# Performance work log

Measured on AMD Instinct MI355X. Metric: run time of the kernel, lower is better.

The kernel has to match this reference:

```python
import jax, jax.numpy as jnp
import numpy as np

B, T, C, L = 256, 256, 1024, 32
NEG = -1e30   # log-domain 'zero'
EPS = 1e-7    # keras.backend.epsilon()


def setup_inputs() -> dict:
    key = jax.random.key(0)
    k1, k2 = jax.random.split(key)
    # ctc_batch_cost expects softmax probabilities
    y_pred = jax.nn.softmax(jax.random.normal(k1, (B, T, C), dtype=jnp.float32), axis=-1)
    # labels in [1, C-2]: 0 is padding (count_nonzero), C-1 is the CTC blank
    y_true = jax.random.randint(k2, (B, L), 1, C - 1).astype(jnp.int32)
    return {"y_true": y_true, "y_pred": y_pred}


def _ctc_batch_cost(y_true, y_pred):
    b, t, c = y_pred.shape
    blank = c - 1                                   # TF ctc_loss: blank = last class
    lp = jnp.log(y_pred + EPS)                      # [B,T,C]
    l = y_true.shape[1]
    s = 2 * l + 1                                   # extended label length
    labels = y_true.astype(jnp.int32)
    # extended label seq: blank, l1, blank, l2, ..., blank
    ext = jnp.full((b, s), blank, jnp.int32).at[:, 1::2].set(labels)  # [B,S]
    label_len = jnp.sum((y_true != 0).astype(jnp.int32), axis=1)      # [B]
    # gather per-step log-probs of extended labels -> [B,T,S]
    lp_ext = jnp.take_along_axis(lp, jnp.broadcast_to(ext[:, None, :], (b, t, s)), axis=2)
    # skip transition s-2 -> s allowed iff ext[s] != blank and ext[s] != ext[s-2]
    prev2 = jnp.concatenate([jnp.full((b, 2), -1, jnp.int32), ext[:, :-2]], axis=1)
    allow_skip = (ext != blank) & (ext != prev2)    # [B,S]

    alpha = jnp.full((b, s), NEG, lp.dtype)
    alpha = alpha.at[:, 0].set(lp_ext[:, 0, 0]).at[:, 1].set(lp_ext[:, 0, 1])
    lp_t = jnp.transpose(lp_ext, (1, 0, 2))         # [T,B,S]

    def step(a, lpt):
        a1 = a
        a2 = jnp.concatenate([jnp.full((b, 1), NEG, a.dtype), a[:, :-1]], axis=1)
        a3 = jnp.concatenate([jnp.full((b, 2), NEG, a.dtype), a[:, :-2]], axis=1)
        a3 = jnp.where(allow_skip, a3, NEG)
        a_new = lpt + jnp.logaddexp(jnp.logaddexp(a1, a2), a3)
        return a_new, None

    alpha, _ = jax.lax.scan(step, alpha, lp_t[1:])  # input_length == T (full)
    bi = jnp.arange(b)
    idx_last_blank = 2 * label_len                  # position 2*Lb (last blank)
    idx_last_label = 2 * label_len - 1
    loss = -jnp.logaddexp(alpha[bi, idx_last_blank], alpha[bi, idx_last_label])
    return loss[:, None]                            # [B,1], matches ctc_batch_cost


def reference(y_true, y_pred):
    return _ctc_batch_cost(y_true, y_pred)
```

## Files before the change

kernel.cpp:

```cpp
#include <hip/hip_runtime.h>
#include <math.h>


#define Bt 256
#define Tt 256
#define Ct 1024
#define Lt 32
#define NSEL 33
#define TOTE (Bt * Tt * NSEL)
#define NEGV (-1e30f)
#define EPSV (1e-7f)

__device__ __forceinline__ float lae2(float a, float b) {
    float m = fmaxf(a, b);
    return m + __logf(__expf(a - m) + __expf(b - m));
}
__device__ __forceinline__ float lae3(float a, float b, float c) {
    float m = fmaxf(fmaxf(a, b), c);
    return m + __logf(__expf(a - m) + __expf(b - m) + __expf(c - m));
}

__global__ __launch_bounds__(256) void ctc_gather(const int* __restrict__ y_true,
                                                  const float* __restrict__ y_pred,
                                                  float* __restrict__ ws) {
    unsigned e = blockIdx.x * 256u + threadIdx.x;
    unsigned row = e / 33u;
    unsigned j = e - row * 33u;
    unsigned b = row >> 8;
    int cls = Ct - 1;
    if (j < 32u) cls = y_true[(b << 5) + j];
    float v = y_pred[((size_t)row << 10) + (unsigned)cls];
    ws[e] = __logf(v + EPSV);
}

__global__ __launch_bounds__(64) void ctc_rec(const int* __restrict__ y_true,
                                              const float* __restrict__ ws,
                                              float* __restrict__ out) {
    const int b = blockIdx.x;
    const int lane = threadIdx.x;
    const int li = (lane < 33) ? lane : 32;
    const float* lp = ws + (size_t)b * Tt * NSEL;
    const int* lab = y_true + b * Lt;

    int cls = (lane < 32) ? lab[lane] : (Ct - 1);
    bool allow = true;
    if (lane >= 1 && lane < 32) {
        int lprev = lab[lane - 1];
        allow = (cls != Ct - 1) && (cls != lprev);
    }
    unsigned long long nz = __ballot(lane < 32 && cls != 0);
    int ll = (int)__popcll(nz);

    float buf[16];
    #pragma unroll
    for (int k = 0; k < 16; ++k) buf[k] = lp[k * NSEL + li];

    float a_even = NEGV, a_odd = NEGV;
    for (int g = 0; g < 16; ++g) {
        #pragma unroll
        for (int k = 0; k < 16; ++k) {
            float cur = buf[k];
            buf[k] = lp[((unsigned)((g + 1) * 16 + k)) * NSEL + li];
            float le = __shfl(cur, 32);
            float lo = (lane < 32) ? cur : NEGV;
            if (k == 0 && g == 0) {
                a_even = (lane == 0) ? le : NEGV;
                a_odd  = (lane == 0) ? lo : NEGV;
            } else {
                float po = __shfl_up(a_odd, 1);
                if (lane == 0) po = NEGV;
                float ne = le + lae2(a_even, po);
                float no = lo + lae3(a_odd, a_even, allow ? po : NEGV);
                a_even = ne;
                a_odd  = no;
            }
        }
    }

    float v1 = __shfl(a_even, ll);
    float v2 = (ll >= 1) ? __shfl(a_odd, ll - 1) : NEGV;
    if (lane == 0) out[b] = -lae2(v1, v2);
}

extern "C" void kernel_launch(void* const* d_in, const int* in_sizes, int n_in,
                              void* d_out, int out_size, void* d_ws, size_t ws_size,
                              hipStream_t stream) {
    const int* y_true = (const int*)d_in[0];
    const float* y_pred = (const float*)d_in[1];
    float* out = (float*)d_out;
    float* ws = (float*)d_ws;
    (void)in_sizes; (void)n_in; (void)out_size; (void)ws_size;
    ctc_gather<<<TOTE / 256, 256, 0, stream>>>(y_true, y_pred, ws);
    ctc_rec<<<Bt, 64, 0, stream>>>(y_true, ws, out);
}
```

Baseline: 373.2 us.

## Stream full y_pred rows coalesced with shared class map instead of scattered gather

```diff
diff --git a/kernel.cpp b/kernel.cpp
--- a/kernel.cpp
+++ b/kernel.cpp
@@ -7,7 +7,7 @@
 #define Ct 1024
 #define Lt 32
 #define NSEL 33
-#define TOTE (Bt * Tt * NSEL)
+#define RPB 16
 #define NEGV (-1e30f)
 #define EPSV (1e-7f)
 
@@ -20,17 +20,45 @@
     return m + __logf(__expf(a - m) + __expf(b - m) + __expf(c - m));
 }
 
-__global__ __launch_bounds__(256) void ctc_gather(const int* __restrict__ y_true,
-                                                  const float* __restrict__ y_pred,
-                                                  float* __restrict__ ws) {
-    unsigned e = blockIdx.x * 256u + threadIdx.x;
-    unsigned row = e / 33u;
-    unsigned j = e - row * 33u;
-    unsigned b = row >> 8;
-    int cls = Ct - 1;
-    if (j < 32u) cls = y_true[(b << 5) + j];
-    float v = y_pred[((size_t)row << 10) + (unsigned)cls];
-    ws[e] = __logf(v + EPSV);
+__global__ __launch_bounds__(256) void ctc_sel(const int* __restrict__ y_true,
+                                               const float* __restrict__ y_pred,
+                                               float* __restrict__ ws) {
+    __shared__ unsigned char map[Ct];
+    const int tid = threadIdx.x;
+    const int b = blockIdx.x >> 4;
+    const int chunk = blockIdx.x & 15;
+
+    ((unsigned*)map)[tid] = 0xFFFFFFFFu;
+    __syncthreads();
+    if (tid == 0) {
+        map[Ct - 1] = 32;
+        const int* lab = y_true + b * Lt;
+        for (int j = Lt - 1; j >= 0; --j)
+            map[lab[j]] = (unsigned char)j;
+    }
+    __syncthreads();
+
+    const float4* src = (const float4*)y_pred
+                      + ((size_t)b * Tt * Ct + (size_t)chunk * RPB * Ct) / 4;
+    float* wsb = ws + ((size_t)b * Tt + (size_t)chunk * RPB) * NSEL;
+
+    #pragma unroll
+    for (int i = 0; i < 16; ++i) {
+        int f = i * 256 + tid;
+        float4 v = src[f];
+        int row = f >> 8;
+        int cbase = (f & 255) << 2;
+        unsigned m4 = *(const unsigned*)(map + cbase);
+        if (m4 != 0xFFFFFFFFu) {
+            float* wr = wsb + row * NSEL;
+            unsigned m0 = m4 & 255u, m1 = (m4 >> 8) & 255u;
+            unsigned m2 = (m4 >> 16) & 255u, m3 = m4 >> 24;
+            if (m0 != 255u) wr[m0] = __logf(v.x + EPSV);
+            if (m1 != 255u) wr[m1] = __logf(v.y + EPSV);
+            if (m2 != 255u) wr[m2] = __logf(v.z + EPSV);
+            if (m3 != 255u) wr[m3] = __logf(v.w + EPSV);
+        }
+    }
 }
 
 __global__ __launch_bounds__(64) void ctc_rec(const int* __restrict__ y_true,
@@ -38,14 +66,20 @@
                                               float* __restrict__ out) {
     const int b = blockIdx.x;
     const int lane = threadIdx.x;
-    const int li = (lane < 33) ? lane : 32;
     const float* lp = ws + (size_t)b * Tt * NSEL;
     const int* lab = y_true + b * Lt;
 
     int cls = (lane < 32) ? lab[lane] : (Ct - 1);
+    int rep = lane;
+    for (int k = 0; k < 32; ++k) {
+        int ck = __shfl(cls, k);
+        if (k < lane && ck == cls && k < rep) rep = k;
+    }
+    const int li = (lane < 32) ? rep : 32;
+
     bool allow = true;
     if (lane >= 1 && lane < 32) {
-        int lprev = lab[lane - 1];
+        int lprev = __shfl(cls, lane - 1);
         allow = (cls != Ct - 1) && (cls != lprev);
     }
     unsigned long long nz = __ballot(lane < 32 && cls != 0);
@@ -90,6 +124,6 @@
     float* out = (float*)d_out;
     float* ws = (float*)d_ws;
     (void)in_sizes; (void)n_in; (void)out_size; (void)ws_size;
-    ctc_gather<<<TOTE / 256, 256, 0, stream>>>(y_true, y_pred, ws);
+    ctc_sel<<<Bt * (Tt / RPB), 256, 0, stream>>>(y_true, y_pred, ws);
     ctc_rec<<<Bt, 64, 0, stream>>>(y_true, ws, out);
 }
```

New measurement: 415.6 us. 1.11x slower.
